# Performance work log

Measured on AMD Instinct MI355X. Metric: run time of the kernel, lower is better.

Reference implementation:

```python
import jax, jax.numpy as jnp
import numpy as np

E = 1024          # embed_dim
BS = 8            # number of sequences (bs = pre_lf_indexs.shape[0])
L = 8192          # tokens per sequence
N = BS * L        # packed tokens
CACHE = 16384     # lf cache rows
EPS = 1e-6


def setup_inputs() -> dict:
    key = jax.random.key(0)
    ks = jax.random.split(key, 9)
    inputs = jax.random.normal(ks[0], (N, E), jnp.float32)
    conv1_weight = jax.random.normal(ks[1], (E, E), jnp.float32) * (1.0 / np.sqrt(E))
    conv2_weight = jax.random.normal(ks[2], (E // 2, 2 * E), jnp.float32) * (1.0 / np.sqrt(E // 2))
    conv1_bias = jax.random.normal(ks[3], (E // 2,), jnp.float32) * 0.02
    conv2_bias = jax.random.normal(ks[4], (E,), jnp.float32) * 0.02
    ln_weight = jnp.ones((E,), jnp.float32)
    lf1_caches = jax.random.normal(ks[5], (CACHE, E), jnp.float32)
    lf2_caches = jax.random.normal(ks[6], (CACHE, E // 2), jnp.float32)
    # packed layout: each sequence prefixed by one cache slot -> T = N + BS rows
    offs = jnp.arange(BS, dtype=jnp.int32) * (L + 1)
    input_lf_loc = offs                                             # cache slot per seq
    inputs_loc = (offs[:, None] + 1 + jnp.arange(L, dtype=jnp.int32)[None, :]).reshape(-1)
    outputs_loc = inputs_loc - 1                                     # 2-tap causal pairing
    out_lf_loc = offs + L                                            # last token of each seq
    pre_lf_indexs = jax.random.randint(ks[7], (BS,), 0, CACHE, jnp.int32)
    out_lf_indexs = jax.random.randint(ks[8], (BS,), 0, CACHE, jnp.int32)
    return {
        'inputs': inputs, 'conv1_weight': conv1_weight, 'conv2_weight': conv2_weight,
        'conv1_bias': conv1_bias, 'conv2_bias': conv2_bias, 'ln_weight': ln_weight,
        'lf1_caches': lf1_caches, 'lf2_caches': lf2_caches,
        'pre_lf_indexs': pre_lf_indexs, 'out_lf_indexs': out_lf_indexs,
        'input_lf_loc': input_lf_loc, 'out_lf_loc': out_lf_loc,
        'inputs_loc': inputs_loc, 'outputs_loc': outputs_loc,
    }


def _fused_cat_conv2d(x, cache, W, pre_idx, in_lf_loc, in_loc, out_loc):
    # scatter cache rows + token rows into the padded buffer [N+bs, D]
    T = x.shape[0] + pre_idx.shape[0]
    xt = jnp.zeros((T, x.shape[1]), x.dtype)
    xt = xt.at[in_lf_loc].set(cache[pre_idx])   # gather from lf cache
    xt = xt.at[in_loc].set(x)
    co = xt @ W                                  # [T, 2*Dout]
    h = co.shape[1] // 2
    # shifted 2-tap causal conv: pair row j (prev) with row j+1 (cur)
    ot = co[:-1, :h] + co[1:, h:]                # [T-1, Dout]
    return ot[out_loc]                           # gather back to token order


def reference(inputs, conv1_weight, conv2_weight, conv1_bias, conv2_bias, ln_weight,
              lf1_caches, lf2_caches, pre_lf_indexs, out_lf_indexs,
              input_lf_loc, out_lf_loc, inputs_loc, outputs_loc):
    # (the index_put_ cache writes in the original are side effects for future
    #  steps only; they do not affect this call's output, so they are omitted)
    output1 = _fused_cat_conv2d(inputs, lf1_caches, conv1_weight,
                                pre_lf_indexs, input_lf_loc, inputs_loc, outputs_loc)
    output1 = output1 + conv1_bias               # [N, E/2]
    output2 = _fused_cat_conv2d(output1, lf2_caches, conv2_weight,
                                pre_lf_indexs, input_lf_loc, inputs_loc, outputs_loc)
    output2 = output2 + conv2_bias               # [N, E]
    x = output2 + inputs                         # residual
    var = jnp.mean(x * x, axis=-1, keepdims=True)
    return x * jax.lax.rsqrt(var + EPS) * ln_weight
```

## Files before the change

### kernel.cpp

```cpp
#include <hip/hip_runtime.h>
#include <hip/hip_bf16.h>


#define EDIM 1024
#define HDIM 512
#define LSEQ 8192
#define BSEQ 8
#define SEQR 8193
#define MTOT (BSEQ * SEQR)
#define MPAD 65792
#define N1 1024
#define N2 2048

using v8s = __attribute__((ext_vector_type(8))) short;
using v4f = __attribute__((ext_vector_type(4))) float;

__device__ __forceinline__ unsigned short f2b(float f) {
  union { float f; unsigned u; } v; v.f = f;
  unsigned r = v.u + 0x7fffu + ((v.u >> 16) & 1u);
  return (unsigned short)(r >> 16);
}
__device__ __forceinline__ float b2f(unsigned short h) {
  union { unsigned u; float f; } v; v.u = ((unsigned)h) << 16; return v.f;
}
__device__ __forceinline__ void gl_lds16(const void* g, void* l) {
  __builtin_amdgcn_global_load_lds((const __attribute__((address_space(1))) void*)g,
                                   (__attribute__((address_space(3))) void*)l, 16, 0, 0);
}

__global__ __launch_bounds__(256) void transpose_cvt(const float* __restrict__ src,
                                                     unsigned short* __restrict__ dst,
                                                     int R, int C) {
  __shared__ float t[64][65];
  const int c0 = blockIdx.x * 64, r0 = blockIdx.y * 64;
  const int tx = threadIdx.x & 63, ty = threadIdx.x >> 6;
#pragma unroll
  for (int yy = 0; yy < 64; yy += 4)
    t[yy + ty][tx] = src[(size_t)(r0 + yy + ty) * C + c0 + tx];
  __syncthreads();
#pragma unroll
  for (int yy = 0; yy < 64; yy += 4)
    dst[(size_t)(c0 + yy + ty) * R + r0 + tx] = f2b(t[tx][yy + ty]);
}

__global__ void prep_small(const float* __restrict__ lf2, const int* __restrict__ preidx,
                           unsigned short* __restrict__ c2b) {
  const int tid = threadIdx.x;
#pragma unroll
  for (int b = 0; b < BSEQ; ++b)
    c2b[b * HDIM + tid] = f2b(lf2[(size_t)preidx[b] * HDIM + tid]);
}

__global__ __launch_bounds__(256) void cvt_full(const float* __restrict__ inputs,
                                                const float* __restrict__ lf1,
                                                const int* __restrict__ preidx,
                                                unsigned short* __restrict__ Xbf) {
  const int r = blockIdx.x * 4 + (threadIdx.x >> 6);
  const int lane = threadIdx.x & 63;
  unsigned short* dst = Xbf + (size_t)r * EDIM;
  if (r >= MTOT) {
#pragma unroll
    for (int c = lane * 4; c < EDIM; c += 256)
      *(ushort4*)&dst[c] = (ushort4){0, 0, 0, 0};
    return;
  }
  const int b = r / SEQR, rr = r % SEQR;
  const float* src = (rr == 0) ? (lf1 + (size_t)preidx[b] * EDIM)
                               : (inputs + (size_t)(b * LSEQ + rr - 1) * EDIM);
#pragma unroll
  for (int c = lane * 4; c < EDIM; c += 256) {
    const float4 v = *(const float4*)(src + c);
    *(ushort4*)&dst[c] = (ushort4){f2b(v.x), f2b(v.y), f2b(v.z), f2b(v.w)};
  }
}

__global__ __launch_bounds__(256) void a2_full(const unsigned short* __restrict__ Z1,
                                               const float* __restrict__ b1,
                                               const unsigned short* __restrict__ c2b,
                                               unsigned short* __restrict__ A2) {
  const int r = blockIdx.x * 4 + (threadIdx.x >> 6);
  const int lane = threadIdx.x & 63;
  unsigned short* dst = A2 + (size_t)r * HDIM;
  if (r >= MTOT) {
#pragma unroll
    for (int c = lane * 4; c < HDIM; c += 256)
      *(ushort4*)&dst[c] = (ushort4){0, 0, 0, 0};
    return;
  }
  const int b = r / SEQR, rr = r % SEQR;
  if (rr == 0) {
#pragma unroll
    for (int c = lane * 4; c < HDIM; c += 256)
      *(ushort4*)&dst[c] = *(const ushort4*)&c2b[b * HDIM + c];
    return;
  }
#pragma unroll
  for (int c = lane * 4; c < HDIM; c += 256) {
    const ushort4 lo = *(const ushort4*)&Z1[(size_t)(r - 1) * N1 + c];
    const ushort4 hi = *(const ushort4*)&Z1[(size_t)r * N1 + HDIM + c];
    const float4 q = *(const float4*)(b1 + c);
    *(ushort4*)&dst[c] = (ushort4){f2b(b2f(lo.x) + b2f(hi.x) + q.x),
                                   f2b(b2f(lo.y) + b2f(hi.y) + q.y),
                                   f2b(b2f(lo.z) + b2f(hi.z) + q.z),
                                   f2b(b2f(lo.w) + b2f(hi.w) + q.w)};
  }
}

#define PHASE(p)                                                                      \
  {                                                                                   \
    v8s af[2][2];                                                                     \
    _Pragma("unroll") for (int m2 = 0; m2 < 2; ++m2)                                  \
    _Pragma("unroll") for (int kx = 0; kx < 2; ++kx)                                  \
      af[m2][kx] = *(const v8s*)&lds[bo + ((2 * (p) + m2) * 32 + wm * 16 + lr) * 64 + \
                                     (((kx * 4 + lk) ^ ra7) << 3)];                   \
    __builtin_amdgcn_s_setprio(1);                                                    \
    _Pragma("unroll") for (int m2 = 0; m2 < 2; ++m2)                                  \
    _Pragma("unroll") for (int nc = 0; nc < 4; ++nc)                                  \
    _Pragma("unroll") for (int kx = 0; kx < 2; ++kx)                                  \
      acc[2 * (p) + m2][nc] = __builtin_amdgcn_mfma_f32_16x16x32_bf16(                \
          af[m2][kx], bf[nc][kx], acc[2 * (p) + m2][nc], 0, 0, 0);                    \
    __builtin_amdgcn_s_setprio(0);                                                    \
  }

#define LOAD_BFR(bo_)                                                                 \
  _Pragma("unroll") for (int nc = 0; nc < 4; ++nc)                                    \
  _Pragma("unroll") for (int kx = 0; kx < 2; ++kx)                                    \
    bf[nc][kx] = *(const v8s*)&lds[(bo_) + 16384 + (nc * 64 + wn * 16 + lr) * 64 +    \
                                   (((kx * 4 + lk) ^ ra7) << 3)];

template <int K, int NT>
__global__ __launch_bounds__(512, 2) void gemm8p(const unsigned short* __restrict__ A,
                                                 const unsigned short* __restrict__ B,
                                                 unsigned short* __restrict__ C,
                                                 int q, int r) {
  __shared__ __align__(16) unsigned short lds[65536];
  constexpr int NTILES = K / 64;
  constexpr int N = NT * 256;
  const int h = blockIdx.x;
  const int xcd = h & 7, idx = h >> 3;
  const int t = (xcd < r ? xcd * (q + 1) : r * (q + 1) + (xcd - r) * q) + idx;
  const int mt = t / NT, nt = t % NT;
  const size_t m0 = (size_t)mt * 256, n0 = (size_t)nt * 256;
  const int tid = threadIdx.x;
  const int w = tid >> 6, lane = tid & 63;
  const int wm = w >> 2, wn = w & 3;
  const int lr = lane & 15, lk = lane >> 4;
  const int ra7 = lr & 7;
  const int srow = tid >> 3, slot = tid & 7;
  const int gslot = slot ^ (srow & 7);
  const unsigned short* aSrc = A + (m0 + srow) * K + gslot * 8;
  const unsigned short* bSrc = B + (n0 + srow) * K + gslot * 8;
  const int dA = srow * 64 + slot * 8;

  auto stageA = [&](int buf, int hh, int tt) {
    const unsigned short* s = aSrc + (size_t)hh * 128 * K + (size_t)tt * 64;
    unsigned short* d = &lds[buf * 32768 + hh * 8192 + dA];
    gl_lds16(s, d);
    gl_lds16(s + (size_t)64 * K, d + 4096);
  };
  auto stageB = [&](int buf, int hh, int tt) {
    const unsigned short* s = bSrc + (size_t)hh * 128 * K + (size_t)tt * 64;
    unsigned short* d = &lds[buf * 32768 + 16384 + hh * 8192 + dA];
    gl_lds16(s, d);
    gl_lds16(s + (size_t)64 * K, d + 4096);
  };

  v4f acc[8][4];
#pragma unroll
  for (int i = 0; i < 8; ++i)
#pragma unroll
    for (int j = 0; j < 4; ++j) acc[i][j] = (v4f){0.f, 0.f, 0.f, 0.f};

  stageB(0, 0, 0); stageB(0, 1, 0); stageA(0, 0, 0); stageA(0, 1, 0);
  asm volatile("s_waitcnt vmcnt(2)" ::: "memory");
  __builtin_amdgcn_s_barrier();

#pragma unroll 2
  for (int t0 = 0; t0 < NTILES - 1; ++t0) {
    const int bo = (t0 & 1) * 32768;
    const int nb = (t0 + 1) & 1;
    v8s bf[4][2];
    stageB(nb, 0, t0 + 1);
    LOAD_BFR(bo)
    PHASE(0)
    stageB(nb, 1, t0 + 1);
    PHASE(1)
    asm volatile("s_waitcnt vmcnt(4)" ::: "memory");
    __builtin_amdgcn_s_barrier();
    stageA(nb, 0, t0 + 1);
    PHASE(2)
    stageA(nb, 1, t0 + 1);
    PHASE(3)
    asm volatile("s_waitcnt vmcnt(2)" ::: "memory");
    __builtin_amdgcn_s_barrier();
  }

  {
    const int bo = ((NTILES - 1) & 1) * 32768;
    v8s bf[4][2];
    LOAD_BFR(bo)
    PHASE(0)
    PHASE(1)
    asm volatile("s_waitcnt vmcnt(0)" ::: "memory");
    __builtin_amdgcn_s_barrier();
    PHASE(2)
    PHASE(3)
  }

#pragma unroll
  for (int mr = 0; mr < 8; ++mr)
#pragma unroll
    for (int nc = 0; nc < 4; ++nc)
#pragma unroll
      for (int g = 0; g < 4; ++g) {
        const size_t row = m0 + mr * 32 + wm * 16 + lk * 4 + g;
        const size_t col = n0 + nc * 64 + wn * 16 + lr;
        C[row * N + col] = f2b(acc[mr][nc][g]);
      }
}

__global__ __launch_bounds__(256) void epilogue_full(
    const unsigned short* __restrict__ Z2, const unsigned short* __restrict__ Xbf,
    const float* __restrict__ b2, const float* __restrict__ lnw,
    float* __restrict__ out) {
  const int g = blockIdx.x;
  const int b = g >> 13, t = g & (LSEQ - 1);
  const size_t r = (size_t)b * SEQR + t;
  const int tid = threadIdx.x;
  const int j0 = tid * 4;

  const ushort4 zl = *(const ushort4*)&Z2[r * N2 + j0];
  const ushort4 zh = *(const ushort4*)&Z2[(r + 1) * N2 + EDIM + j0];
  const ushort4 xb = *(const ushort4*)&Xbf[(r + 1) * EDIM + j0];
  const float4 bb = *(const float4*)&b2[j0];
  const float4 lw = *(const float4*)&lnw[j0];

  const float x0 = b2f(zl.x) + b2f(zh.x) + bb.x + b2f(xb.x);
  const float x1 = b2f(zl.y) + b2f(zh.y) + bb.y + b2f(xb.y);
  const float x2 = b2f(zl.z) + b2f(zh.z) + bb.z + b2f(xb.z);
  const float x3 = b2f(zl.w) + b2f(zh.w) + bb.w + b2f(xb.w);

  float ss = x0 * x0 + x1 * x1 + x2 * x2 + x3 * x3;
#pragma unroll
  for (int o = 32; o > 0; o >>= 1) ss += __shfl_xor(ss, o, 64);
  __shared__ float sp[4];
  if ((tid & 63) == 0) sp[tid >> 6] = ss;
  __syncthreads();
  const float tot = sp[0] + sp[1] + sp[2] + sp[3];
  const float scale = rsqrtf(tot * (1.0f / EDIM) + 1e-6f);

  float4 o4;
  o4.x = x0 * scale * lw.x; o4.y = x1 * scale * lw.y;
  o4.z = x2 * scale * lw.z; o4.w = x3 * scale * lw.w;
  *(float4*)&out[(size_t)(b * LSEQ + t) * EDIM + j0] = o4;
}

extern "C" void kernel_launch(void* const* d_in, const int* in_sizes, int n_in,
                              void* d_out, int out_size, void* d_ws, size_t ws_size,
                              hipStream_t stream) {
  const float* inputs = (const float*)d_in[0];
  const float* W1 = (const float*)d_in[1];
  const float* W2 = (const float*)d_in[2];
  const float* b1 = (const float*)d_in[3];
  const float* b2 = (const float*)d_in[4];
  const float* lnw = (const float*)d_in[5];
  const float* lf1 = (const float*)d_in[6];
  const float* lf2 = (const float*)d_in[7];
  const int* preidx = (const int*)d_in[8];
  float* out = (float*)d_out;

  char* ws = (char*)d_ws;
  unsigned short* Xbf = (unsigned short*)(ws);
  unsigned short* Z1  = (unsigned short*)(ws + 134742016ULL);
  unsigned short* A2  = (unsigned short*)(ws + 269484032ULL);
  unsigned short* Z2  = (unsigned short*)(ws + 336855040ULL);
  unsigned short* W1T = (unsigned short*)(ws + 606339072ULL);
  unsigned short* W2T = (unsigned short*)(ws + 608436224ULL);
  unsigned short* c2b = (unsigned short*)(ws + 610533376ULL);

  transpose_cvt<<<dim3(16, 16), 256, 0, stream>>>(W1, W1T, 1024, 1024);
  transpose_cvt<<<dim3(32, 8), 256, 0, stream>>>(W2, W2T, 512, 2048);
  prep_small<<<1, 512, 0, stream>>>(lf2, preidx, c2b);

  cvt_full<<<MPAD / 4, 256, 0, stream>>>(inputs, lf1, preidx, Xbf);
  gemm8p<1024, 4><<<1028, 512, 0, stream>>>(Xbf, W1T, Z1, 128, 4);
  a2_full<<<MPAD / 4, 256, 0, stream>>>(Z1, b1, c2b, A2);
  gemm8p<512, 8><<<2056, 512, 0, stream>>>(A2, W2T, Z2, 257, 0);
  epilogue_full<<<BSEQ * LSEQ, 256, 0, stream>>>(Z2, Xbf, b2, lnw, out);
}
```

Measured before the change: 546.8 us.

## Fold 2-tap conv shift into K-concatenated GEMMs, drop intermediate combine passes

Each 2-tap causal conv is recast as one GEMM with K doubled: A rows are read as overlapping pairs (row j and j+1, LDA smaller than K) and the weight halves are concatenated along K. The output is only half as wide and is written directly in shifted token order with bias fused in. This removes the a2_full combine kernel and halves Z1/Z2 output traffic, and the epilogue now reads a single Z row. The GEMM also gets a 3-stage A ring buffer with more LDS, which may lower occupancy or change the pipeline timing.

Result: faster. 470.9 us (-13.9%).

```diff
diff --git a/kernel.cpp b/kernel.cpp
--- a/kernel.cpp
+++ b/kernel.cpp
@@ -9,8 +9,7 @@
 #define SEQR 8193
 #define MTOT (BSEQ * SEQR)
 #define MPAD 65792
-#define N1 1024
-#define N2 2048
+#define XROWS 66048
 
 using v8s = __attribute__((ext_vector_type(8))) short;
 using v4f = __attribute__((ext_vector_type(4))) float;
@@ -28,19 +27,19 @@
                                    (__attribute__((address_space(3))) void*)l, 16, 0, 0);
 }
 
-__global__ __launch_bounds__(256) void transpose_cvt(const float* __restrict__ src,
-                                                     unsigned short* __restrict__ dst,
-                                                     int R, int C) {
+__global__ __launch_bounds__(256) void transpose_cat(const float* __restrict__ src, int src_ld,
+                                                     int src_c0, unsigned short* __restrict__ dst,
+                                                     int dst_ld, int dst_k0) {
   __shared__ float t[64][65];
-  const int c0 = blockIdx.x * 64, r0 = blockIdx.y * 64;
+  const int n0 = blockIdx.x * 64, k0 = blockIdx.y * 64;
   const int tx = threadIdx.x & 63, ty = threadIdx.x >> 6;
 #pragma unroll
   for (int yy = 0; yy < 64; yy += 4)
-    t[yy + ty][tx] = src[(size_t)(r0 + yy + ty) * C + c0 + tx];
+    t[yy + ty][tx] = src[(size_t)(k0 + yy + ty) * src_ld + src_c0 + n0 + tx];
   __syncthreads();
 #pragma unroll
   for (int yy = 0; yy < 64; yy += 4)
-    dst[(size_t)(c0 + yy + ty) * R + r0 + tx] = f2b(t[tx][yy + ty]);
+    dst[(size_t)(n0 + yy + ty) * dst_ld + dst_k0 + k0 + tx] = f2b(t[tx][yy + ty]);
 }
 
 __global__ void prep_small(const float* __restrict__ lf2, const int* __restrict__ preidx,
@@ -74,72 +73,49 @@
   }
 }
 
-__global__ __launch_bounds__(256) void a2_full(const unsigned short* __restrict__ Z1,
-                                               const float* __restrict__ b1,
-                                               const unsigned short* __restrict__ c2b,
-                                               unsigned short* __restrict__ A2) {
-  const int r = blockIdx.x * 4 + (threadIdx.x >> 6);
-  const int lane = threadIdx.x & 63;
-  unsigned short* dst = A2 + (size_t)r * HDIM;
-  if (r >= MTOT) {
-#pragma unroll
-    for (int c = lane * 4; c < HDIM; c += 256)
-      *(ushort4*)&dst[c] = (ushort4){0, 0, 0, 0};
-    return;
-  }
-  const int b = r / SEQR, rr = r % SEQR;
-  if (rr == 0) {
-#pragma unroll
-    for (int c = lane * 4; c < HDIM; c += 256)
-      *(ushort4*)&dst[c] = *(const ushort4*)&c2b[b * HDIM + c];
-    return;
-  }
-#pragma unroll
-  for (int c = lane * 4; c < HDIM; c += 256) {
-    const ushort4 lo = *(const ushort4*)&Z1[(size_t)(r - 1) * N1 + c];
-    const ushort4 hi = *(const ushort4*)&Z1[(size_t)r * N1 + HDIM + c];
-    const float4 q = *(const float4*)(b1 + c);
-    *(ushort4*)&dst[c] = (ushort4){f2b(b2f(lo.x) + b2f(hi.x) + q.x),
-                                   f2b(b2f(lo.y) + b2f(hi.y) + q.y),
-                                   f2b(b2f(lo.z) + b2f(hi.z) + q.z),
-                                   f2b(b2f(lo.w) + b2f(hi.w) + q.w)};
-  }
-}
-
-#define PHASE(p)                                                                      \
-  {                                                                                   \
-    v8s af[2][2];                                                                     \
-    _Pragma("unroll") for (int m2 = 0; m2 < 2; ++m2)                                  \
-    _Pragma("unroll") for (int kx = 0; kx < 2; ++kx)                                  \
-      af[m2][kx] = *(const v8s*)&lds[bo + ((2 * (p) + m2) * 32 + wm * 16 + lr) * 64 + \
-                                     (((kx * 4 + lk) ^ ra7) << 3)];                   \
-    __builtin_amdgcn_s_setprio(1);                                                    \
-    _Pragma("unroll") for (int m2 = 0; m2 < 2; ++m2)                                  \
-    _Pragma("unroll") for (int nc = 0; nc < 4; ++nc)                                  \
-    _Pragma("unroll") for (int kx = 0; kx < 2; ++kx)                                  \
-      acc[2 * (p) + m2][nc] = __builtin_amdgcn_mfma_f32_16x16x32_bf16(                \
-          af[m2][kx], bf[nc][kx], acc[2 * (p) + m2][nc], 0, 0, 0);                    \
-    __builtin_amdgcn_s_setprio(0);                                                    \
-  }
-
-#define LOAD_BFR(bo_)                                                                 \
-  _Pragma("unroll") for (int nc = 0; nc < 4; ++nc)                                    \
-  _Pragma("unroll") for (int kx = 0; kx < 2; ++kx)                                    \
-    bf[nc][kx] = *(const v8s*)&lds[(bo_) + 16384 + (nc * 64 + wn * 16 + lr) * 64 +    \
+__global__ void fixup_a2(const unsigned short* __restrict__ c2b,
+                         unsigned short* __restrict__ A2) {
+  const int tid = threadIdx.x;
+#pragma unroll
+  for (int b = 0; b < BSEQ; ++b)
+    A2[(size_t)(b * SEQR) * HDIM + tid] = c2b[b * HDIM + tid];
+}
+
+#define PHASE(p, boA_)                                                                 \
+  {                                                                                    \
+    v8s af[2][2];                                                                      \
+    _Pragma("unroll") for (int m2 = 0; m2 < 2; ++m2)                                   \
+    _Pragma("unroll") for (int kx = 0; kx < 2; ++kx)                                   \
+      af[m2][kx] = *(const v8s*)&lds[(boA_) + ((2 * (p) + m2) * 32 + wm * 16 + lr) * 64 + \
+                                     (((kx * 4 + lk) ^ ra7) << 3)];                    \
+    __builtin_amdgcn_s_setprio(1);                                                     \
+    _Pragma("unroll") for (int m2 = 0; m2 < 2; ++m2)                                   \
+    _Pragma("unroll") for (int nc = 0; nc < 4; ++nc)                                   \
+    _Pragma("unroll") for (int kx = 0; kx < 2; ++kx)                                   \
+      acc[2 * (p) + m2][nc] = __builtin_amdgcn_mfma_f32_16x16x32_bf16(                 \
+          af[m2][kx], bf[nc][kx], acc[2 * (p) + m2][nc], 0, 0, 0);                     \
+    __builtin_amdgcn_s_setprio(0);                                                     \
+  }
+
+#define LOAD_BFR(boB_)                                                                 \
+  _Pragma("unroll") for (int nc = 0; nc < 4; ++nc)                                     \
+  _Pragma("unroll") for (int kx = 0; kx < 2; ++kx)                                     \
+    bf[nc][kx] = *(const v8s*)&lds[(boB_) + (nc * 64 + wn * 16 + lr) * 64 +            \
                                    (((kx * 4 + lk) ^ ra7) << 3)];
 
-template <int K, int NT>
-__global__ __launch_bounds__(512, 2) void gemm8p(const unsigned short* __restrict__ A,
+template <int K, int LDA, int NT, bool AMAP, bool SHIFTC>
+__global__ __launch_bounds__(512, 2) void gemm3b(const unsigned short* __restrict__ A,
                                                  const unsigned short* __restrict__ B,
                                                  unsigned short* __restrict__ C,
+                                                 const float* __restrict__ bias,
                                                  int q, int r) {
-  __shared__ __align__(16) unsigned short lds[65536];
+  __shared__ __align__(16) unsigned short lds[81920];
   constexpr int NTILES = K / 64;
   constexpr int N = NT * 256;
   const int h = blockIdx.x;
   const int xcd = h & 7, idx = h >> 3;
-  const int t = (xcd < r ? xcd * (q + 1) : r * (q + 1) + (xcd - r) * q) + idx;
-  const int mt = t / NT, nt = t % NT;
+  const int tsw = (xcd < r ? xcd * (q + 1) : r * (q + 1) + (xcd - r) * q) + idx;
+  const int mt = tsw / NT, nt = tsw % NT;
   const size_t m0 = (size_t)mt * 256, n0 = (size_t)nt * 256;
   const int tid = threadIdx.x;
   const int w = tid >> 6, lane = tid & 63;
@@ -148,22 +124,24 @@
   const int ra7 = lr & 7;
   const int srow = tid >> 3, slot = tid & 7;
   const int gslot = slot ^ (srow & 7);
-  const unsigned short* aSrc = A + (m0 + srow) * K + gslot * 8;
-  const unsigned short* bSrc = B + (n0 + srow) * K + gslot * 8;
   const int dA = srow * 64 + slot * 8;
-
-  auto stageA = [&](int buf, int hh, int tt) {
-    const unsigned short* s = aSrc + (size_t)hh * 128 * K + (size_t)tt * 64;
-    unsigned short* d = &lds[buf * 32768 + hh * 8192 + dA];
+  const unsigned short* bSrc = B + (size_t)(n0 + srow) * K + gslot * 8;
+
+  auto stageA = [&](int dst, int hh, int tt) {
+#pragma unroll
+    for (int hf = 0; hf < 2; ++hf) {
+      int u = (int)m0 + hh * 128 + hf * 64 + srow;
+      if constexpr (AMAP) u += (u >> 13);
+      gl_lds16(A + (size_t)u * LDA + tt * 64 + gslot * 8,
+               &lds[dst + hh * 8192 + hf * 4096 + dA]);
+    }
+  };
+  auto stageB = [&](int dst, int hh, int tt) {
+    const unsigned short* s = bSrc + (size_t)hh * 128 * K + (size_t)tt * 64;
+    unsigned short* d = &lds[dst + hh * 8192 + dA];
     gl_lds16(s, d);
     gl_lds16(s + (size_t)64 * K, d + 4096);
   };
-  auto stageB = [&](int buf, int hh, int tt) {
-    const unsigned short* s = bSrc + (size_t)hh * 128 * K + (size_t)tt * 64;
-    unsigned short* d = &lds[buf * 32768 + 16384 + hh * 8192 + dA];
-    gl_lds16(s, d);
-    gl_lds16(s + (size_t)64 * K, d + 4096);
-  };
 
   v4f acc[8][4];
 #pragma unroll
@@ -171,74 +149,85 @@
 #pragma unroll
     for (int j = 0; j < 4; ++j) acc[i][j] = (v4f){0.f, 0.f, 0.f, 0.f};
 
-  stageB(0, 0, 0); stageB(0, 1, 0); stageA(0, 0, 0); stageA(0, 1, 0);
-  asm volatile("s_waitcnt vmcnt(2)" ::: "memory");
+  stageB(49152, 0, 0); stageB(49152, 1, 0);
+  stageA(0, 0, 0);     stageA(0, 1, 0);
+  stageA(16384, 0, 1); stageA(16384, 1, 1);
+  asm volatile("s_waitcnt vmcnt(4)" ::: "memory");
   __builtin_amdgcn_s_barrier();
 
-#pragma unroll 2
-  for (int t0 = 0; t0 < NTILES - 1; ++t0) {
-    const int bo = (t0 & 1) * 32768;
-    const int nb = (t0 + 1) & 1;
+  int boA = 0, soA = 32768;
+  int boB = 49152, sB = 65536;
+#pragma unroll 1
+  for (int t0 = 0; t0 < NTILES - 2; ++t0) {
     v8s bf[4][2];
-    stageB(nb, 0, t0 + 1);
-    LOAD_BFR(bo)
-    PHASE(0)
-    stageB(nb, 1, t0 + 1);
-    PHASE(1)
+    stageB(sB, 0, t0 + 1);
+    LOAD_BFR(boB)
+    PHASE(0, boA)
+    stageB(sB, 1, t0 + 1);
+    PHASE(1, boA)
+    stageA(soA, 0, t0 + 2);
+    PHASE(2, boA)
+    stageA(soA, 1, t0 + 2);
+    PHASE(3, boA)
     asm volatile("s_waitcnt vmcnt(4)" ::: "memory");
     __builtin_amdgcn_s_barrier();
-    stageA(nb, 0, t0 + 1);
-    PHASE(2)
-    stageA(nb, 1, t0 + 1);
-    PHASE(3)
-    asm volatile("s_waitcnt vmcnt(2)" ::: "memory");
-    __builtin_amdgcn_s_barrier();
-  }
-
+    const int nboA = (boA == 32768) ? 0 : boA + 16384;
+    soA = boA; boA = nboA;
+    const int tmp = boB; boB = sB; sB = tmp;
+  }
   {
-    const int bo = ((NTILES - 1) & 1) * 32768;
     v8s bf[4][2];
-    LOAD_BFR(bo)
-    PHASE(0)
-    PHASE(1)
+    stageB(sB, 0, NTILES - 1);
+    LOAD_BFR(boB)
+    PHASE(0, boA)
+    stageB(sB, 1, NTILES - 1);
+    PHASE(1, boA)
+    PHASE(2, boA)
+    PHASE(3, boA)
     asm volatile("s_waitcnt vmcnt(0)" ::: "memory");
     __builtin_amdgcn_s_barrier();
-    PHASE(2)
-    PHASE(3)
+    boA = (boA == 32768) ? 0 : boA + 16384;
+    const int tmp = boB; boB = sB; sB = tmp;
+  }
+  {
+    v8s bf[4][2];
+    LOAD_BFR(boB)
+    PHASE(0, boA) PHASE(1, boA) PHASE(2, boA) PHASE(3, boA)
   }
 
 #pragma unroll
   for (int mr = 0; mr < 8; ++mr)
 #pragma unroll
-    for (int nc = 0; nc < 4; ++nc)
+    for (int nc = 0; nc < 4; ++nc) {
+      const size_t col = n0 + nc * 64 + wn * 16 + lr;
+      float bv = 0.f;
+      if constexpr (SHIFTC) bv = bias[col];
 #pragma unroll
       for (int g = 0; g < 4; ++g) {
-        const size_t row = m0 + mr * 32 + wm * 16 + lk * 4 + g;
-        const size_t col = n0 + nc * 64 + wn * 16 + lr;
-        C[row * N + col] = f2b(acc[mr][nc][g]);
+        const size_t row = m0 + mr * 32 + wm * 16 + lk * 4 + g + (SHIFTC ? 1 : 0);
+        C[row * N + col] = f2b(acc[mr][nc][g] + bv);
       }
+    }
 }
 
 __global__ __launch_bounds__(256) void epilogue_full(
-    const unsigned short* __restrict__ Z2, const unsigned short* __restrict__ Xbf,
+    const unsigned short* __restrict__ Zo, const unsigned short* __restrict__ Xbf,
     const float* __restrict__ b2, const float* __restrict__ lnw,
     float* __restrict__ out) {
-  const int g = blockIdx.x;
-  const int b = g >> 13, t = g & (LSEQ - 1);
-  const size_t r = (size_t)b * SEQR + t;
+  const int u = blockIdx.x;
+  const size_t rx = (size_t)u + (u >> 13) + 1;
   const int tid = threadIdx.x;
   const int j0 = tid * 4;
 
-  const ushort4 zl = *(const ushort4*)&Z2[r * N2 + j0];
-  const ushort4 zh = *(const ushort4*)&Z2[(r + 1) * N2 + EDIM + j0];
-  const ushort4 xb = *(const ushort4*)&Xbf[(r + 1) * EDIM + j0];
+  const ushort4 z = *(const ushort4*)&Zo[(size_t)u * EDIM + j0];
+  const ushort4 xb = *(const ushort4*)&Xbf[rx * EDIM + j0];
   const float4 bb = *(const float4*)&b2[j0];
   const float4 lw = *(const float4*)&lnw[j0];
 
-  const float x0 = b2f(zl.x) + b2f(zh.x) + bb.x + b2f(xb.x);
-  const float x1 = b2f(zl.y) + b2f(zh.y) + bb.y + b2f(xb.y);
-  const float x2 = b2f(zl.z) + b2f(zh.z) + bb.z + b2f(xb.z);
-  const float x3 = b2f(zl.w) + b2f(zh.w) + bb.w + b2f(xb.w);
+  const float x0 = b2f(z.x) + bb.x + b2f(xb.x);
+  const float x1 = b2f(z.y) + bb.y + b2f(xb.y);
+  const float x2 = b2f(z.z) + bb.z + b2f(xb.z);
+  const float x3 = b2f(z.w) + bb.w + b2f(xb.w);
 
   float ss = x0 * x0 + x1 * x1 + x2 * x2 + x3 * x3;
 #pragma unroll
@@ -252,7 +241,7 @@
   float4 o4;
   o4.x = x0 * scale * lw.x; o4.y = x1 * scale * lw.y;
   o4.z = x2 * scale * lw.z; o4.w = x3 * scale * lw.w;
-  *(float4*)&out[(size_t)(b * LSEQ + t) * EDIM + j0] = o4;
+  *(float4*)&out[(size_t)u * EDIM + j0] = o4;
 }
 
 extern "C" void kernel_launch(void* const* d_in, const int* in_sizes, int n_in,
@@ -271,20 +260,21 @@
 
   char* ws = (char*)d_ws;
   unsigned short* Xbf = (unsigned short*)(ws);
-  unsigned short* Z1  = (unsigned short*)(ws + 134742016ULL);
-  unsigned short* A2  = (unsigned short*)(ws + 269484032ULL);
-  unsigned short* Z2  = (unsigned short*)(ws + 336855040ULL);
-  unsigned short* W1T = (unsigned short*)(ws + 606339072ULL);
-  unsigned short* W2T = (unsigned short*)(ws + 608436224ULL);
-  unsigned short* c2b = (unsigned short*)(ws + 610533376ULL);
-
-  transpose_cvt<<<dim3(16, 16), 256, 0, stream>>>(W1, W1T, 1024, 1024);
-  transpose_cvt<<<dim3(32, 8), 256, 0, stream>>>(W2, W2T, 512, 2048);
+  unsigned short* A2  = (unsigned short*)(ws + 135266304ULL);
+  unsigned short* Zo  = (unsigned short*)(ws + 202899456ULL);
+  unsigned short* W1c = (unsigned short*)(ws + 337117184ULL);
+  unsigned short* W2c = (unsigned short*)(ws + 339214336ULL);
+  unsigned short* c2b = (unsigned short*)(ws + 341311488ULL);
+
+  transpose_cat<<<dim3(8, 16), 256, 0, stream>>>(W1, 1024, 0, W1c, 2048, 0);
+  transpose_cat<<<dim3(8, 16), 256, 0, stream>>>(W1, 1024, 512, W1c, 2048, 1024);
+  transpose_cat<<<dim3(16, 8), 256, 0, stream>>>(W2, 2048, 0, W2c, 1024, 0);
+  transpose_cat<<<dim3(16, 8), 256, 0, stream>>>(W2, 2048, 1024, W2c, 1024, 512);
   prep_small<<<1, 512, 0, stream>>>(lf2, preidx, c2b);
 
-  cvt_full<<<MPAD / 4, 256, 0, stream>>>(inputs, lf1, preidx, Xbf);
-  gemm8p<1024, 4><<<1028, 512, 0, stream>>>(Xbf, W1T, Z1, 128, 4);
-  a2_full<<<MPAD / 4, 256, 0, stream>>>(Z1, b1, c2b, A2);
-  gemm8p<512, 8><<<2056, 512, 0, stream>>>(A2, W2T, Z2, 257, 0);
-  epilogue_full<<<BSEQ * LSEQ, 256, 0, stream>>>(Z2, Xbf, b2, lnw, out);
-}
+  cvt_full<<<XROWS / 4, 256, 0, stream>>>(inputs, lf1, preidx, Xbf);
+  gemm3b<2048, 1024, 2, false, true><<<514, 512, 0, stream>>>(Xbf, W1c, A2, b1, 64, 2);
+  fixup_a2<<<1, 512, 0, stream>>>(c2b, A2);
+  gemm3b<1024, 512, 4, true, false><<<1024, 512, 0, stream>>>(A2, W2c, Zo, nullptr, 128, 0);
+  epilogue_full<<<BSEQ * LSEQ, 256, 0, stream>>>(Zo, Xbf, b2, lnw, out);
+}
```
